# Optimization experiments

Hardware: AMD Instinct MI355X
Metric: run time of the kernel (lower is better)

The kernel has to match this reference:

```python
import math
import jax, jax.numpy as jnp
import numpy as np

B, S, D = 1, 2048, 4096
H, KVH, HD = 32, 8, 128  # head_dim = D // H; n_rep = H // KVH = 4
MAXB, MAXS = 1, 2048
ROPE_THETA = 10000.0


def setup_inputs() -> dict:
    key = jax.random.key(0)
    ks = jax.random.split(key, 6)
    x = jax.random.normal(ks[0], (B, S, D), dtype=jnp.float32)
    sc = 0.02
    wq = jax.random.normal(ks[1], (D, H * HD), dtype=jnp.float32) * sc
    wk = jax.random.normal(ks[2], (D, KVH * HD), dtype=jnp.float32) * sc
    wv = jax.random.normal(ks[3], (D, KVH * HD), dtype=jnp.float32) * sc
    wo = jax.random.normal(ks[4], (H * HD, D), dtype=jnp.float32) * sc
    # rotary phases: freqs_cis[t, j] = exp(i * t * theta^(-2j/hd))
    inv_freq = 1.0 / (ROPE_THETA ** (jnp.arange(0, HD, 2, dtype=jnp.float32) / HD))
    ang = jnp.arange(S, dtype=jnp.float32)[:, None] * inv_freq[None, :]  # [S, HD//2]
    freqs_cos = jnp.cos(ang)
    freqs_sin = jnp.sin(ang)
    # causal additive mask over the cache window (start_pos=0 prefill)
    mask = jnp.where(jnp.triu(jnp.ones((S, S), dtype=bool), k=1), -1e9, 0.0).astype(jnp.float32)
    cache_k = jnp.zeros((MAXB, MAXS, KVH, HD), dtype=jnp.float32)
    cache_v = jnp.zeros((MAXB, MAXS, KVH, HD), dtype=jnp.float32)
    return {"x": x, "wq": wq, "wk": wk, "wv": wv, "wo": wo,
            "freqs_cos": freqs_cos, "freqs_sin": freqs_sin, "mask": mask,
            "cache_k": cache_k, "cache_v": cache_v, "start_pos": 0}


def _apply_rope(t, cos, sin):
    # t: [B, S, h, HD]; cos/sin: [S, HD//2]
    te, to = t[..., ::2], t[..., 1::2]
    cos = cos[None, :, None, :]
    sin = sin[None, :, None, :]
    out = jnp.stack([te * cos - to * sin, to * cos + te * sin], axis=-1)
    return out.reshape(t.shape)


def _repeat_kv(t, n_rep):
    # faithful to source: rep axis inserted before kv-head axis
    bs, slen, n_kv, hd = t.shape
    if n_rep == 1:
        return t
    return jnp.repeat(t[:, :, None, :, :], n_rep, axis=2).reshape(bs, slen, n_kv * n_rep, hd)


def reference(x, wq, wk, wv, wo, freqs_cos, freqs_sin, mask, cache_k, cache_v, start_pos):
    bsz, seqlen, _ = x.shape
    n_rep = H // KVH
    xq = (x @ wq).reshape(bsz, seqlen, H, HD)
    xk = (x @ wk).reshape(bsz, seqlen, KVH, HD)
    xv = (x @ wv).reshape(bsz, seqlen, KVH, HD)
    xq = _apply_rope(xq, freqs_cos, freqs_sin)
    xk = _apply_rope(xk, freqs_cos, freqs_sin)
    # KV-cache append
    cache_k = cache_k.at[:bsz, start_pos:start_pos + seqlen].set(xk)
    cache_v = cache_v.at[:bsz, start_pos:start_pos + seqlen].set(xv)
    keys = _repeat_kv(cache_k[:bsz, :start_pos + seqlen], n_rep)    # [B, T, H, HD]
    values = _repeat_kv(cache_v[:bsz, :start_pos + seqlen], n_rep)  # [B, T, H, HD]
    scores = jnp.einsum('bqhd,bkhd->bhqk', xq, keys) / math.sqrt(HD)
    scores = scores + mask[None, None, :, :]
    probs = jax.nn.softmax(scores, axis=-1)
    out = jnp.einsum('bhqk,bkhd->bqhd', probs, values).reshape(bsz, seqlen, H * HD)
    return out @ wo
```

## Files before the change

### kernel.cpp

```cpp
#include <hip/hip_runtime.h>
#include <stdint.h>


using bf16x8 = __attribute__((ext_vector_type(8))) short;
using f32x4  = __attribute__((ext_vector_type(4))) float;
using s16x4  = __attribute__((ext_vector_type(4))) short;

__device__ __forceinline__ short f2bf(float f) {
    union { float f; unsigned u; } v; v.f = f;
    unsigned r = v.u + 0x7fffu + ((v.u >> 16) & 1u);
    return (short)(r >> 16);
}
__device__ __forceinline__ float bf2f(short s) {
    union { unsigned u; float f; } v; v.u = ((unsigned)(unsigned short)s) << 16;
    return v.f;
}

#define GLL16(gp, lp)                                                          \
    __builtin_amdgcn_global_load_lds(                                          \
        (const __attribute__((address_space(1))) void*)(gp),                   \
        (__attribute__((address_space(3))) void*)(lp), 16, 0, 0)

__global__ __launch_bounds__(256) void cvt_f32_bf16(const float* __restrict__ x,
                                                    short* __restrict__ y, int n) {
    int i = (blockIdx.x * 256 + threadIdx.x) * 4;
    if (i >= n) return;
    f32x4 v = *(const f32x4*)(x + i);
    s16x4 o;
    o.x = f2bf(v.x); o.y = f2bf(v.y); o.z = f2bf(v.z); o.w = f2bf(v.w);
    *(s16x4*)(y + i) = o;
}

__global__ __launch_bounds__(256) void transpose_f32_bf16(const float* __restrict__ W,
                                                          short* __restrict__ WT,
                                                          int K, int N) {
    __shared__ float t[32][33];
    int n0 = blockIdx.x * 32, k0 = blockIdx.y * 32;
    int tx = threadIdx.x, ty = threadIdx.y;
#pragma unroll
    for (int i = 0; i < 32; i += 8)
        t[ty + i][tx] = W[(size_t)(k0 + ty + i) * N + n0 + tx];
    __syncthreads();
#pragma unroll
    for (int i = 0; i < 32; i += 8)
        WT[(size_t)(n0 + ty + i) * K + k0 + tx] = f2bf(t[tx][ty + i]);
}

__global__ __launch_bounds__(256) void transpose_bf16(const short* __restrict__ A,
                                                      short* __restrict__ AT,
                                                      int R, int C, int lda) {
    __shared__ short t[32][33];
    int c0 = blockIdx.x * 32, r0 = blockIdx.y * 32;
    int tx = threadIdx.x, ty = threadIdx.y;
#pragma unroll
    for (int i = 0; i < 32; i += 8)
        t[ty + i][tx] = A[(size_t)(r0 + ty + i) * lda + c0 + tx];
    __syncthreads();
#pragma unroll
    for (int i = 0; i < 32; i += 8)
        AT[(size_t)(c0 + ty + i) * R + r0 + tx] = t[tx][ty + i];
}

__global__ __launch_bounds__(256) void gemm_bf16(const short* __restrict__ A,
                                                 const short* __restrict__ BT,
                                                 float* __restrict__ Cf,
                                                 short* __restrict__ Cb,
                                                 int M, int N, int K) {
    __shared__ short As[128 * 32];
    __shared__ short Bs[128 * 32];
    const int tid  = threadIdx.x;
    const int wave = tid >> 6, lane = tid & 63;
    const int lrow = lane & 15, quad = lane >> 4, lk8 = quad * 8;
    const int bm = blockIdx.y * 128, bn = blockIdx.x * 128;
    const int wm = (wave >> 1) * 64, wn = (wave & 1) * 64;

    f32x4 acc[4][4];
#pragma unroll
    for (int i = 0; i < 4; i++)
#pragma unroll
        for (int j = 0; j < 4; j++) acc[i][j] = (f32x4){0.f, 0.f, 0.f, 0.f};

    for (int k0 = 0; k0 < K; k0 += 32) {
        __syncthreads();
#pragma unroll
        for (int s = 0; s < 2; s++) {
            int idx = tid * 8 + s * 2048;
            int row = idx >> 5, col = idx & 31;
            GLL16(A  + (size_t)(bm + row) * K + k0 + col, &As[idx]);
            GLL16(BT + (size_t)(bn + row) * K + k0 + col, &Bs[idx]);
        }
        __syncthreads();
        bf16x8 af[4], bfr[4];
#pragma unroll
        for (int i = 0; i < 4; i++) af[i]  = *(const bf16x8*)&As[(wm + i * 16 + lrow) * 32 + lk8];
#pragma unroll
        for (int j = 0; j < 4; j++) bfr[j] = *(const bf16x8*)&Bs[(wn + j * 16 + lrow) * 32 + lk8];
#pragma unroll
        for (int i = 0; i < 4; i++)
#pragma unroll
            for (int j = 0; j < 4; j++)
                acc[i][j] = __builtin_amdgcn_mfma_f32_16x16x32_bf16(af[i], bfr[j], acc[i][j], 0, 0, 0);
    }

#pragma unroll
    for (int i = 0; i < 4; i++)
#pragma unroll
        for (int j = 0; j < 4; j++)
#pragma unroll
            for (int r = 0; r < 4; r++) {
                int m = bm + wm + i * 16 + quad * 4 + r;
                int n = bn + wn + j * 16 + lrow;
                float v = acc[i][j][r];
                if (Cf) Cf[(size_t)m * N + n] = v;
                else    Cb[(size_t)m * N + n] = f2bf(v);
            }
}

__global__ __launch_bounds__(256) void rope_kernel(short* __restrict__ q,
                                                   short* __restrict__ kv,
                                                   const float* __restrict__ fc,
                                                   const float* __restrict__ fs) {
    int s = blockIdx.x, t = threadIdx.x;
#pragma unroll
    for (int p = t; p < 2048; p += 256) {
        int i = p & 63;
        float c = fc[s * 64 + i], sn = fs[s * 64 + i];
        int base = s * 4096 + 2 * p;
        float e = bf2f(q[base]), o = bf2f(q[base + 1]);
        q[base]     = f2bf(e * c - o * sn);
        q[base + 1] = f2bf(o * c + e * sn);
    }
#pragma unroll
    for (int p = t; p < 512; p += 256) {
        int i = p & 63;
        float c = fc[s * 64 + i], sn = fs[s * 64 + i];
        int base = s * 2048 + 2 * p;
        float e = bf2f(kv[base]), o = bf2f(kv[base + 1]);
        kv[base]     = f2bf(e * c - o * sn);
        kv[base + 1] = f2bf(o * c + e * sn);
    }
}

#define KSLD 136
#define VSLD 40
__global__ __launch_bounds__(256) void attn_kernel(const short* __restrict__ Q,
                                                   const short* __restrict__ KV,
                                                   const short* __restrict__ VT,
                                                   short* __restrict__ AO) {
    const int qb = 63 - blockIdx.x;
    const int kvh = blockIdx.y;
    const int wave = threadIdx.x >> 6, lane = threadIdx.x & 63;
    const int lrow = lane & 15, quad = lane >> 4, lk8 = quad * 8;
    const int h = wave * 8 + kvh;
    const int q0 = qb * 32;

    __shared__ short Ks[32 * KSLD];
    __shared__ short Vs[128 * VSLD];
    __shared__ short Pw[4][2][16 * 32];

    bf16x8 aq[2][4];
#pragma unroll
    for (int rs = 0; rs < 2; rs++) {
        const short* qrow = Q + (size_t)(q0 + rs * 16 + lrow) * 4096 + h * 128;
#pragma unroll
        for (int f = 0; f < 4; f++) aq[rs][f] = *(const bf16x8*)(qrow + f * 32 + lk8);
    }

    f32x4 o_acc[2][8];
#pragma unroll
    for (int rs = 0; rs < 2; rs++)
#pragma unroll
        for (int d = 0; d < 8; d++) o_acc[rs][d] = (f32x4){0.f, 0.f, 0.f, 0.f};
    float l_part[2][4];
#pragma unroll
    for (int rs = 0; rs < 2; rs++)
#pragma unroll
        for (int r = 0; r < 4; r++) l_part[rs][r] = 0.f;

    const int nkt = qb + 1;
    const float sc = 0.08838834764831845f;

    for (int kt = 0; kt < nkt; kt++) {
        __syncthreads();
#pragma unroll
        for (int c = 0; c < 2; c++) {
            int idx = (threadIdx.x + c * 256) * 8;
            int key = idx >> 7, d = idx & 127;
            *(bf16x8*)&Ks[key * KSLD + d] =
                *(const bf16x8*)(KV + (size_t)(kt * 32 + key) * 2048 + kvh * 128 + d);
            int dr = idx >> 5, kc = idx & 31;
            *(bf16x8*)&Vs[dr * VSLD + kc] =
                *(const bf16x8*)(VT + (size_t)(kvh * 128 + dr) * 2048 + kt * 32 + kc);
        }
        __syncthreads();

        f32x4 s0[2], s1[2];
#pragma unroll
        for (int rs = 0; rs < 2; rs++) { s0[rs] = (f32x4){0.f,0.f,0.f,0.f}; s1[rs] = s0[rs]; }
#pragma unroll
        for (int f = 0; f < 4; f++) {
            bf16x8 b0 = *(const bf16x8*)&Ks[(lrow)      * KSLD + f * 32 + lk8];
            bf16x8 b1 = *(const bf16x8*)&Ks[(16 + lrow) * KSLD + f * 32 + lk8];
#pragma unroll
            for (int rs = 0; rs < 2; rs++) {
                s0[rs] = __builtin_amdgcn_mfma_f32_16x16x32_bf16(aq[rs][f], b0, s0[rs], 0, 0, 0);
                s1[rs] = __builtin_amdgcn_mfma_f32_16x16x32_bf16(aq[rs][f], b1, s1[rs], 0, 0, 0);
            }
        }

        int keyg0 = kt * 32 + lrow, keyg1 = keyg0 + 16;
#pragma unroll
        for (int rs = 0; rs < 2; rs++)
#pragma unroll
            for (int r = 0; r < 4; r++) {
                int qg = q0 + rs * 16 + quad * 4 + r;
                float p0 = (keyg0 > qg) ? 0.f : __expf(s0[rs][r] * sc);
                float p1 = (keyg1 > qg) ? 0.f : __expf(s1[rs][r] * sc);
                l_part[rs][r] += p0 + p1;
                Pw[wave][rs][(quad * 4 + r) * 32 + lrow]      = f2bf(p0);
                Pw[wave][rs][(quad * 4 + r) * 32 + 16 + lrow] = f2bf(p1);
            }

#pragma unroll
        for (int rs = 0; rs < 2; rs++) {
            bf16x8 ap = *(const bf16x8*)&Pw[wave][rs][lrow * 32 + lk8];
#pragma unroll
            for (int dt = 0; dt < 8; dt++) {
                bf16x8 bv = *(const bf16x8*)&Vs[(dt * 16 + lrow) * VSLD + lk8];
                o_acc[rs][dt] = __builtin_amdgcn_mfma_f32_16x16x32_bf16(ap, bv, o_acc[rs][dt], 0, 0, 0);
            }
        }
    }

#pragma unroll
    for (int rs = 0; rs < 2; rs++)
#pragma unroll
        for (int r = 0; r < 4; r++) {
            float l = l_part[rs][r];
#pragma unroll
            for (int off = 1; off < 16; off <<= 1) l += __shfl_xor(l, off, 64);
            float inv = 1.f / l;
#pragma unroll
            for (int dt = 0; dt < 8; dt++) {
                int qg = q0 + rs * 16 + quad * 4 + r;
                AO[(size_t)qg * 4096 + h * 128 + dt * 16 + lrow] =
                    f2bf(o_acc[rs][dt][r] * inv);
            }
        }
}

extern "C" void kernel_launch(void* const* d_in, const int* in_sizes, int n_in,
                              void* d_out, int out_size, void* d_ws, size_t ws_size,
                              hipStream_t stream) {
    (void)in_sizes; (void)n_in; (void)out_size; (void)ws_size;
    const float* x  = (const float*)d_in[0];
    const float* wq = (const float*)d_in[1];
    const float* wk = (const float*)d_in[2];
    const float* wv = (const float*)d_in[3];
    const float* wo = (const float*)d_in[4];
    const float* fc = (const float*)d_in[5];
    const float* fs = (const float*)d_in[6];
    float* out = (float*)d_out;

    char* ws = (char*)d_ws;
    size_t off = 0;
    auto carve = [&](size_t bytes) { char* p = ws + off; off = (off + bytes + 255) & ~(size_t)255; return p; };
    short* xb   = (short*)carve(2048u * 4096u * 2);
    short* wqT  = (short*)carve(4096u * 4096u * 2);
    short* wkvT = (short*)carve(2048u * 4096u * 2);
    short* woT  = (short*)carve(4096u * 4096u * 2);
    short* qb   = (short*)carve(2048u * 4096u * 2);
    short* kvb  = (short*)carve(2048u * 2048u * 2);
    short* vtb  = (short*)carve(1024u * 2048u * 2);
    short* aob  = xb;

    dim3 tb(32, 8);
    cvt_f32_bf16<<<8192, 256, 0, stream>>>(x, xb, 2048 * 4096);
    transpose_f32_bf16<<<dim3(128, 128), tb, 0, stream>>>(wq, wqT, 4096, 4096);
    transpose_f32_bf16<<<dim3(32, 128),  tb, 0, stream>>>(wk, wkvT, 4096, 1024);
    transpose_f32_bf16<<<dim3(32, 128),  tb, 0, stream>>>(wv, wkvT + (size_t)1024 * 4096, 4096, 1024);
    transpose_f32_bf16<<<dim3(128, 128), tb, 0, stream>>>(wo, woT, 4096, 4096);

    gemm_bf16<<<dim3(32, 16), 256, 0, stream>>>(xb, wqT,  nullptr, qb,  2048, 4096, 4096);
    gemm_bf16<<<dim3(16, 16), 256, 0, stream>>>(xb, wkvT, nullptr, kvb, 2048, 2048, 4096);

    rope_kernel<<<2048, 256, 0, stream>>>(qb, kvb, fc, fs);
    transpose_bf16<<<dim3(32, 64), tb, 0, stream>>>(kvb + 1024, vtb, 2048, 1024, 2048);

    attn_kernel<<<dim3(64, 8), 256, 0, stream>>>(qb, kvb, vtb, aob);

    gemm_bf16<<<dim3(32, 16), 256, 0, stream>>>(aob, woT, out, nullptr, 2048, 4096, 4096);
}
```

Before: 668.8 us.

## Fuse QKV projection, widen GEMM and attention K-tiles, vectorize weight transpose

Merges the Q and KV projection GEMMs into one QKV GEMM over a concatenated transposed weight, so the layout becomes a single [S,6144] buffer and one launch replaces two. The GEMM k-step doubles to 64 (two 32-wide LDS panels per sync), halving barrier count. Attention processes 64 keys per tile instead of 32, with padded LDS strides for P and V. The weight transpose now handles 64 rows per block and writes packed 32-bit bf16 pairs. These add LDS usage and register pressure, and the 64-key tile may do extra masked work on the causal diagonal.

```diff
diff --git a/kernel.cpp b/kernel.cpp
--- a/kernel.cpp
+++ b/kernel.cpp
@@ -34,16 +34,20 @@
 __global__ __launch_bounds__(256) void transpose_f32_bf16(const float* __restrict__ W,
                                                           short* __restrict__ WT,
                                                           int K, int N) {
-    __shared__ float t[32][33];
-    int n0 = blockIdx.x * 32, k0 = blockIdx.y * 32;
+    __shared__ float t[64][33];
+    int n0 = blockIdx.x * 32, k0 = blockIdx.y * 64;
     int tx = threadIdx.x, ty = threadIdx.y;
 #pragma unroll
-    for (int i = 0; i < 32; i += 8)
+    for (int i = 0; i < 64; i += 8)
         t[ty + i][tx] = W[(size_t)(k0 + ty + i) * N + n0 + tx];
     __syncthreads();
 #pragma unroll
-    for (int i = 0; i < 32; i += 8)
-        WT[(size_t)(n0 + ty + i) * K + k0 + tx] = f2bf(t[tx][ty + i]);
+    for (int i = 0; i < 32; i += 8) {
+        int n = ty + i;
+        unsigned lo = (unsigned short)f2bf(t[2 * tx][n]);
+        unsigned hi = (unsigned short)f2bf(t[2 * tx + 1][n]);
+        *(unsigned*)&WT[(size_t)(n0 + n) * K + k0 + 2 * tx] = lo | (hi << 16);
+    }
 }
 
 __global__ __launch_bounds__(256) void transpose_bf16(const short* __restrict__ A,
@@ -66,8 +70,8 @@
                                                  float* __restrict__ Cf,
                                                  short* __restrict__ Cb,
                                                  int M, int N, int K) {
-    __shared__ short As[128 * 32];
-    __shared__ short Bs[128 * 32];
+    __shared__ short As[2 * 128 * 32];
+    __shared__ short Bs[2 * 128 * 32];
     const int tid  = threadIdx.x;
     const int wave = tid >> 6, lane = tid & 63;
     const int lrow = lane & 15, quad = lane >> 4, lk8 = quad * 8;
@@ -80,26 +84,32 @@
 #pragma unroll
         for (int j = 0; j < 4; j++) acc[i][j] = (f32x4){0.f, 0.f, 0.f, 0.f};
 
-    for (int k0 = 0; k0 < K; k0 += 32) {
+    for (int k0 = 0; k0 < K; k0 += 64) {
         __syncthreads();
 #pragma unroll
-        for (int s = 0; s < 2; s++) {
+        for (int s = 0; s < 4; s++) {
             int idx = tid * 8 + s * 2048;
-            int row = idx >> 5, col = idx & 31;
+            int panel = idx >> 12, rem = idx & 4095;
+            int row = rem >> 5, col = (panel << 5) + (rem & 31);
             GLL16(A  + (size_t)(bm + row) * K + k0 + col, &As[idx]);
             GLL16(BT + (size_t)(bn + row) * K + k0 + col, &Bs[idx]);
         }
         __syncthreads();
-        bf16x8 af[4], bfr[4];
-#pragma unroll
-        for (int i = 0; i < 4; i++) af[i]  = *(const bf16x8*)&As[(wm + i * 16 + lrow) * 32 + lk8];
-#pragma unroll
-        for (int j = 0; j < 4; j++) bfr[j] = *(const bf16x8*)&Bs[(wn + j * 16 + lrow) * 32 + lk8];
-#pragma unroll
-        for (int i = 0; i < 4; i++)
+#pragma unroll
+        for (int p = 0; p < 2; p++) {
+            bf16x8 af[4], bfr[4];
+#pragma unroll
+            for (int i = 0; i < 4; i++)
+                af[i]  = *(const bf16x8*)&As[p * 4096 + (wm + i * 16 + lrow) * 32 + lk8];
 #pragma unroll
             for (int j = 0; j < 4; j++)
-                acc[i][j] = __builtin_amdgcn_mfma_f32_16x16x32_bf16(af[i], bfr[j], acc[i][j], 0, 0, 0);
+                bfr[j] = *(const bf16x8*)&Bs[p * 4096 + (wn + j * 16 + lrow) * 32 + lk8];
+#pragma unroll
+            for (int i = 0; i < 4; i++)
+#pragma unroll
+                for (int j = 0; j < 4; j++)
+                    acc[i][j] = __builtin_amdgcn_mfma_f32_16x16x32_bf16(af[i], bfr[j], acc[i][j], 0, 0, 0);
+        }
     }
 
 #pragma unroll
@@ -116,8 +126,7 @@
             }
 }
 
-__global__ __launch_bounds__(256) void rope_kernel(short* __restrict__ q,
-                                                   short* __restrict__ kv,
+__global__ __launch_bounds__(256) void rope_kernel(short* __restrict__ qkv,
                                                    const float* __restrict__ fc,
                                                    const float* __restrict__ fs) {
     int s = blockIdx.x, t = threadIdx.x;
@@ -125,26 +134,26 @@
     for (int p = t; p < 2048; p += 256) {
         int i = p & 63;
         float c = fc[s * 64 + i], sn = fs[s * 64 + i];
-        int base = s * 4096 + 2 * p;
-        float e = bf2f(q[base]), o = bf2f(q[base + 1]);
-        q[base]     = f2bf(e * c - o * sn);
-        q[base + 1] = f2bf(o * c + e * sn);
+        size_t base = (size_t)s * 6144 + 2 * p;
+        float e = bf2f(qkv[base]), o = bf2f(qkv[base + 1]);
+        qkv[base]     = f2bf(e * c - o * sn);
+        qkv[base + 1] = f2bf(o * c + e * sn);
     }
 #pragma unroll
     for (int p = t; p < 512; p += 256) {
         int i = p & 63;
         float c = fc[s * 64 + i], sn = fs[s * 64 + i];
-        int base = s * 2048 + 2 * p;
-        float e = bf2f(kv[base]), o = bf2f(kv[base + 1]);
-        kv[base]     = f2bf(e * c - o * sn);
-        kv[base + 1] = f2bf(o * c + e * sn);
+        size_t base = (size_t)s * 6144 + 4096 + 2 * p;
+        float e = bf2f(qkv[base]), o = bf2f(qkv[base + 1]);
+        qkv[base]     = f2bf(e * c - o * sn);
+        qkv[base + 1] = f2bf(o * c + e * sn);
     }
 }
 
 #define KSLD 136
-#define VSLD 40
-__global__ __launch_bounds__(256) void attn_kernel(const short* __restrict__ Q,
-                                                   const short* __restrict__ KV,
+#define VSLD 68
+#define PSLD 68
+__global__ __launch_bounds__(256) void attn_kernel(const short* __restrict__ QKV,
                                                    const short* __restrict__ VT,
                                                    short* __restrict__ AO) {
     const int qb = 63 - blockIdx.x;
@@ -154,14 +163,14 @@
     const int h = wave * 8 + kvh;
     const int q0 = qb * 32;
 
-    __shared__ short Ks[32 * KSLD];
+    __shared__ short Ks[64 * KSLD];
     __shared__ short Vs[128 * VSLD];
-    __shared__ short Pw[4][2][16 * 32];
+    __shared__ short Pw[4][2][16 * PSLD];
 
     bf16x8 aq[2][4];
 #pragma unroll
     for (int rs = 0; rs < 2; rs++) {
-        const short* qrow = Q + (size_t)(q0 + rs * 16 + lrow) * 4096 + h * 128;
+        const short* qrow = QKV + (size_t)(q0 + rs * 16 + lrow) * 6144 + h * 128;
 #pragma unroll
         for (int f = 0; f < 4; f++) aq[rs][f] = *(const bf16x8*)(qrow + f * 32 + lk8);
     }
@@ -177,57 +186,65 @@
 #pragma unroll
         for (int r = 0; r < 4; r++) l_part[rs][r] = 0.f;
 
-    const int nkt = qb + 1;
+    const int nkt = (qb + 2) >> 1;
     const float sc = 0.08838834764831845f;
+    const short* Kbase = QKV + 4096;
 
     for (int kt = 0; kt < nkt; kt++) {
         __syncthreads();
 #pragma unroll
-        for (int c = 0; c < 2; c++) {
+        for (int c = 0; c < 4; c++) {
             int idx = (threadIdx.x + c * 256) * 8;
             int key = idx >> 7, d = idx & 127;
             *(bf16x8*)&Ks[key * KSLD + d] =
-                *(const bf16x8*)(KV + (size_t)(kt * 32 + key) * 2048 + kvh * 128 + d);
-            int dr = idx >> 5, kc = idx & 31;
+                *(const bf16x8*)(Kbase + (size_t)(kt * 64 + key) * 6144 + kvh * 128 + d);
+            int dr = idx >> 6, kc = idx & 63;
             *(bf16x8*)&Vs[dr * VSLD + kc] =
-                *(const bf16x8*)(VT + (size_t)(kvh * 128 + dr) * 2048 + kt * 32 + kc);
+                *(const bf16x8*)(VT + (size_t)(kvh * 128 + dr) * 2048 + kt * 64 + kc);
         }
         __syncthreads();
 
-        f32x4 s0[2], s1[2];
-#pragma unroll
-        for (int rs = 0; rs < 2; rs++) { s0[rs] = (f32x4){0.f,0.f,0.f,0.f}; s1[rs] = s0[rs]; }
-#pragma unroll
-        for (int f = 0; f < 4; f++) {
-            bf16x8 b0 = *(const bf16x8*)&Ks[(lrow)      * KSLD + f * 32 + lk8];
-            bf16x8 b1 = *(const bf16x8*)&Ks[(16 + lrow) * KSLD + f * 32 + lk8];
-#pragma unroll
-            for (int rs = 0; rs < 2; rs++) {
-                s0[rs] = __builtin_amdgcn_mfma_f32_16x16x32_bf16(aq[rs][f], b0, s0[rs], 0, 0, 0);
-                s1[rs] = __builtin_amdgcn_mfma_f32_16x16x32_bf16(aq[rs][f], b1, s1[rs], 0, 0, 0);
-            }
-        }
-
-        int keyg0 = kt * 32 + lrow, keyg1 = keyg0 + 16;
+        f32x4 sacc[2][4];
 #pragma unroll
         for (int rs = 0; rs < 2; rs++)
 #pragma unroll
-            for (int r = 0; r < 4; r++) {
-                int qg = q0 + rs * 16 + quad * 4 + r;
-                float p0 = (keyg0 > qg) ? 0.f : __expf(s0[rs][r] * sc);
-                float p1 = (keyg1 > qg) ? 0.f : __expf(s1[rs][r] * sc);
-                l_part[rs][r] += p0 + p1;
-                Pw[wave][rs][(quad * 4 + r) * 32 + lrow]      = f2bf(p0);
-                Pw[wave][rs][(quad * 4 + r) * 32 + 16 + lrow] = f2bf(p1);
-            }
-
-#pragma unroll
-        for (int rs = 0; rs < 2; rs++) {
-            bf16x8 ap = *(const bf16x8*)&Pw[wave][rs][lrow * 32 + lk8];
+            for (int ks = 0; ks < 4; ks++) sacc[rs][ks] = (f32x4){0.f, 0.f, 0.f, 0.f};
+#pragma unroll
+        for (int ks = 0; ks < 4; ks++)
+#pragma unroll
+            for (int f = 0; f < 4; f++) {
+                bf16x8 bk = *(const bf16x8*)&Ks[(ks * 16 + lrow) * KSLD + f * 32 + lk8];
+#pragma unroll
+                for (int rs = 0; rs < 2; rs++)
+                    sacc[rs][ks] = __builtin_amdgcn_mfma_f32_16x16x32_bf16(aq[rs][f], bk, sacc[rs][ks], 0, 0, 0);
+            }
+
+#pragma unroll
+        for (int rs = 0; rs < 2; rs++)
+#pragma unroll
+            for (int ks = 0; ks < 4; ks++) {
+                int keyg = kt * 64 + ks * 16 + lrow;
+#pragma unroll
+                for (int r = 0; r < 4; r++) {
+                    int qg = q0 + rs * 16 + quad * 4 + r;
+                    float p = (keyg > qg) ? 0.f : __expf(sacc[rs][ks][r] * sc);
+                    l_part[rs][r] += p;
+                    Pw[wave][rs][(quad * 4 + r) * PSLD + ks * 16 + lrow] = f2bf(p);
+                }
+            }
+
+#pragma unroll
+        for (int kp = 0; kp < 2; kp++) {
+            bf16x8 ap[2];
+#pragma unroll
+            for (int rs = 0; rs < 2; rs++)
+                ap[rs] = *(const bf16x8*)&Pw[wave][rs][lrow * PSLD + kp * 32 + lk8];
 #pragma unroll
             for (int dt = 0; dt < 8; dt++) {
-                bf16x8 bv = *(const bf16x8*)&Vs[(dt * 16 + lrow) * VSLD + lk8];
-                o_acc[rs][dt] = __builtin_amdgcn_mfma_f32_16x16x32_bf16(ap, bv, o_acc[rs][dt], 0, 0, 0);
+                bf16x8 bv = *(const bf16x8*)&Vs[(dt * 16 + lrow) * VSLD + kp * 32 + lk8];
+#pragma unroll
+                for (int rs = 0; rs < 2; rs++)
+                    o_acc[rs][dt] = __builtin_amdgcn_mfma_f32_16x16x32_bf16(ap[rs], bv, o_acc[rs][dt], 0, 0, 0);
             }
         }
     }
@@ -265,29 +282,26 @@
     char* ws = (char*)d_ws;
     size_t off = 0;
     auto carve = [&](size_t bytes) { char* p = ws + off; off = (off + bytes + 255) & ~(size_t)255; return p; };
-    short* xb   = (short*)carve(2048u * 4096u * 2);
-    short* wqT  = (short*)carve(4096u * 4096u * 2);
-    short* wkvT = (short*)carve(2048u * 4096u * 2);
-    short* woT  = (short*)carve(4096u * 4096u * 2);
-    short* qb   = (short*)carve(2048u * 4096u * 2);
-    short* kvb  = (short*)carve(2048u * 2048u * 2);
-    short* vtb  = (short*)carve(1024u * 2048u * 2);
-    short* aob  = xb;
+    short* xb    = (short*)carve(2048u * 4096u * 2);
+    short* wqkvT = (short*)carve(6144u * 4096u * 2);
+    short* woT   = (short*)carve(4096u * 4096u * 2);
+    short* qkvb  = (short*)carve(2048u * 6144u * 2);
+    short* vtb   = (short*)carve(1024u * 2048u * 2);
+    short* aob   = xb;
 
     dim3 tb(32, 8);
     cvt_f32_bf16<<<8192, 256, 0, stream>>>(x, xb, 2048 * 4096);
-    transpose_f32_bf16<<<dim3(128, 128), tb, 0, stream>>>(wq, wqT, 4096, 4096);
-    transpose_f32_bf16<<<dim3(32, 128),  tb, 0, stream>>>(wk, wkvT, 4096, 1024);
-    transpose_f32_bf16<<<dim3(32, 128),  tb, 0, stream>>>(wv, wkvT + (size_t)1024 * 4096, 4096, 1024);
-    transpose_f32_bf16<<<dim3(128, 128), tb, 0, stream>>>(wo, woT, 4096, 4096);
-
-    gemm_bf16<<<dim3(32, 16), 256, 0, stream>>>(xb, wqT,  nullptr, qb,  2048, 4096, 4096);
-    gemm_bf16<<<dim3(16, 16), 256, 0, stream>>>(xb, wkvT, nullptr, kvb, 2048, 2048, 4096);
-
-    rope_kernel<<<2048, 256, 0, stream>>>(qb, kvb, fc, fs);
-    transpose_bf16<<<dim3(32, 64), tb, 0, stream>>>(kvb + 1024, vtb, 2048, 1024, 2048);
-
-    attn_kernel<<<dim3(64, 8), 256, 0, stream>>>(qb, kvb, vtb, aob);
+    transpose_f32_bf16<<<dim3(128, 64), tb, 0, stream>>>(wq, wqkvT, 4096, 4096);
+    transpose_f32_bf16<<<dim3(32, 64),  tb, 0, stream>>>(wk, wqkvT + (size_t)4096 * 4096, 4096, 1024);
+    transpose_f32_bf16<<<dim3(32, 64),  tb, 0, stream>>>(wv, wqkvT + (size_t)5120 * 4096, 4096, 1024);
+    transpose_f32_bf16<<<dim3(128, 64), tb, 0, stream>>>(wo, woT, 4096, 4096);
+
+    gemm_bf16<<<dim3(48, 16), 256, 0, stream>>>(xb, wqkvT, nullptr, qkvb, 2048, 6144, 4096);
+
+    rope_kernel<<<2048, 256, 0, stream>>>(qkvb, fc, fs);
+    transpose_bf16<<<dim3(32, 64), tb, 0, stream>>>(qkvb + 5120, vtb, 2048, 1024, 6144);
+
+    attn_kernel<<<dim3(64, 8), 256, 0, stream>>>(qkvb, vtb, aob);
 
     gemm_bf16<<<dim3(32, 16), 256, 0, stream>>>(aob, woT, out, nullptr, 2048, 4096, 4096);
 }
```

Result: no change. 671.2 us (+0.4%).
